# Kernel tuning notes

Hardware: AMD Instinct MI355X
Metric: run time of the kernel (lower is better)

Reference implementation:

```python
import jax, jax.numpy as jnp
import numpy as np

B, T, N_ITEMS, DIM, L = 512, 50, 10000, 128, 4
H = DIM // 2


def setup_inputs() -> dict:
    key = jax.random.key(0)
    ks = jax.random.split(key, 16)
    emb = jax.random.normal(ks[0], (N_ITEMS + 1, DIM), jnp.float32) * 0.02
    emb = emb.at[0].set(0.0)  # padding_idx=0
    s = 1.0 / np.sqrt(DIM)
    inp = {
        "users": jax.random.randint(ks[1], (B,), 0, B),
        "user_seq": jax.random.randint(ks[2], (B, T), 0, N_ITEMS + 1),
        "pos_items": jax.random.randint(ks[3], (B,), 0, N_ITEMS),
        "neg_items": jax.random.randint(ks[4], (B, 10), 0, N_ITEMS),
        "pos_labels": jnp.ones((B,), jnp.float32),
        "neg_labels": jnp.zeros((B, 10), jnp.float32),
        "base_model_preds": jax.random.normal(ks[5], (B, N_ITEMS), jnp.float32),
        "emb": emb,
        "lstm_wih": jax.random.uniform(ks[6], (4 * DIM, DIM), jnp.float32, -s, s),
        "lstm_whh": jax.random.uniform(ks[7], (4 * DIM, DIM), jnp.float32, -s, s),
        "lstm_bih": jax.random.uniform(ks[8], (4 * DIM,), jnp.float32, -s, s),
        "lstm_bhh": jax.random.uniform(ks[9], (4 * DIM,), jnp.float32, -s, s),
        "wl_W1": jax.random.normal(ks[10], (L, 2 * DIM, H), jnp.float32) * 0.05,
        "wl_b1": jax.random.normal(ks[11], (L, H), jnp.float32) * 0.01,
        "wl_W2": jax.random.normal(ks[12], (L, H), jnp.float32) * 0.05,
        "wl_b2": jax.random.normal(ks[13], (L,), jnp.float32) * 0.01,
        "alphas": jnp.ones((L,), jnp.float32) / L,
    }
    return inp


def _lstm_last(x, wih, whh, bih, bhh):
    # x: [B, T, D]; torch gate order i, f, g, o. Returns last hidden state [B, D].
    Bx, _, D = x.shape
    bias = bih + bhh

    def step(carry, xt):
        h, c = carry
        gates = xt @ wih.T + h @ whh.T + bias  # [B, 4D]
        i, f, g, o = jnp.split(gates, 4, axis=-1)
        c = jax.nn.sigmoid(f) * c + jax.nn.sigmoid(i) * jnp.tanh(g)
        h = jax.nn.sigmoid(o) * jnp.tanh(c)
        return (h, c), None

    init = (jnp.zeros((Bx, D), x.dtype), jnp.zeros((Bx, D), x.dtype))
    (h, _), _ = jax.lax.scan(step, init, x.transpose(1, 0, 2))
    return h


def reference(users, user_seq, pos_items, neg_items, pos_labels, neg_labels,
              base_model_preds, emb, lstm_wih, lstm_whh, lstm_bih, lstm_bhh,
              wl_W1, wl_b1, wl_W2, wl_b2, alphas):
    seq_emb = emb[user_seq]                      # [B, T, D]
    seq_repr = _lstm_last(seq_emb, lstm_wih, lstm_whh, lstm_bih, lstm_bhh)  # [B, D]
    item_emb = emb[jnp.arange(N_ITEMS)]          # [N, D]

    # Weak learners: Linear(2D->H) split algebraically into seq/item matmuls
    # to avoid materializing the [B, N, 2D] broadcast-concat tensor.
    final_scores = jnp.zeros((seq_repr.shape[0], N_ITEMS), seq_repr.dtype)
    for l in range(L):
        sp = seq_repr @ wl_W1[l, :DIM]           # [B, H]
        ip = item_emb @ wl_W1[l, DIM:]           # [N, H]
        hid = jax.nn.relu(sp[:, None, :] + ip[None, :, :] + wl_b1[l])  # [B, N, H]
        scores = hid @ wl_W2[l] + wl_b2[l]       # [B, N]
        final_scores = final_scores + alphas[l] * scores

    pos_scores = jnp.take_along_axis(final_scores, pos_items[:, None], axis=1)  # [B, 1]
    neg_scores = jnp.take_along_axis(final_scores, neg_items, axis=1)           # [B, n_neg]
    loss = jnp.mean(jnp.exp(-(pos_scores - neg_scores)))
    return final_scores, loss
```

## Files before the change

kernel.cpp:

```cpp
#include <hip/hip_runtime.h>
#include <stdint.h>

typedef uint32_t u32;
typedef uint16_t u16;
typedef uint64_t u64;
typedef __attribute__((ext_vector_type(4))) float f32x4;
typedef __attribute__((ext_vector_type(8))) short bf16x8;
typedef __attribute__((ext_vector_type(2))) _Float16 f16x2;

#define NI   10000
#define NPAD 10240
#define L2E  1.4426950408889634f

#define DEV static __device__ __forceinline__

DEV float asf(u32 u){ union{u32 i; float f;} v; v.i=u; return v.f; }
DEV u32   asu(float f){ union{u32 i; float f;} v; v.f=f; return v.i; }
DEV float bf2f(u16 u){ return asf(((u32)u)<<16); }
DEV u16   f2bf(float f){ u32 i = asu(f); return (u16)((i + 0x7fffu + ((i>>16)&1u))>>16); }
DEV u16   f2h(float f){ _Float16 h = (_Float16)f; return __builtin_bit_cast(u16, h); }
DEV f32x4 fzero(){ f32x4 z; z[0]=0.f; z[1]=0.f; z[2]=0.f; z[3]=0.f; return z; }

DEV void gl2lds16(const void* g, void* l){
  __builtin_amdgcn_global_load_lds((const __attribute__((address_space(1))) u32*)g,
                                   (__attribute__((address_space(3))) u32*)l, 16, 0, 0);
}

__global__ void k_prep(const int* __restrict__ seq, const float* __restrict__ emb,
                       const float* __restrict__ wih, const float* __restrict__ bih,
                       const float* __restrict__ bhh, const float* __restrict__ W1,
                       const float* __restrict__ b1, const float* __restrict__ W2,
                       const float* __restrict__ alphas,
                       u16* __restrict__ EMB16, u16* __restrict__ Wih16,
                       u16* __restrict__ W1s16, u16* __restrict__ W1i16,
                       float* __restrict__ bias512, float* __restrict__ b1k,
                       float* __restrict__ w2h, u32* __restrict__ w2p,
                       float* __restrict__ qv)
{
  const int tid = blockIdx.x*blockDim.x + threadIdx.x;
  const int nth = gridDim.x*blockDim.x;
  for (int e = tid; e < 10001*16; e += nth){
    const float* s = emb + (size_t)e*8;
    float4 x0 = *(const float4*)s, x1 = *(const float4*)(s+4);
    bf16x8 o;
    o[0]=(short)f2bf(x0.x); o[1]=(short)f2bf(x0.y); o[2]=(short)f2bf(x0.z); o[3]=(short)f2bf(x0.w);
    o[4]=(short)f2bf(x1.x); o[5]=(short)f2bf(x1.y); o[6]=(short)f2bf(x1.z); o[7]=(short)f2bf(x1.w);
    *(bf16x8*)&EMB16[(size_t)e*8] = o;
  }
  for (int e = tid; e < 512*16; e += nth){
    int col = (e*8)>>7;
    float sc = ((col>>7)==2) ? 2.0f*L2E : L2E;
    const float* s = wih + (size_t)e*8;
    float4 x0 = *(const float4*)s, x1 = *(const float4*)(s+4);
    bf16x8 o;
    o[0]=(short)f2bf(x0.x*sc); o[1]=(short)f2bf(x0.y*sc); o[2]=(short)f2bf(x0.z*sc); o[3]=(short)f2bf(x0.w*sc);
    o[4]=(short)f2bf(x1.x*sc); o[5]=(short)f2bf(x1.y*sc); o[6]=(short)f2bf(x1.z*sc); o[7]=(short)f2bf(x1.w*sc);
    *(bf16x8*)&Wih16[(size_t)e*8] = o;
  }
  for (int e = tid; e < 256*128; e += nth){ int k = e>>7, d = e&127; int l = k>>6, h = k&63;
      W1s16[e] = f2bf(W1[l*16384 + d*64 + h]); }
  for (int e = tid; e < 256*128; e += nth){ int k = e>>7, d = e&127; int l = k>>6, h = k&63;
      W1i16[e] = f2bf(W1[l*16384 + (128+d)*64 + h]); }
  for (int e = tid; e < 512; e += nth){
      float sc = ((e>>7)==2) ? 2.0f*L2E : L2E;
      bias512[e] = (bih[e] + bhh[e])*sc; }
  for (int e = tid; e < 256; e += nth){ int l = e>>6, h = e&63;
      b1k[e] = b1[l*64 + h]; w2h[e] = 0.5f*alphas[l]*W2[l*64 + h]; }
  for (int e = tid; e < 128; e += nth){
      int k0 = 2*e, k1 = 2*e+1;
      float w0 = 0.5f*alphas[k0>>6]*W2[(k0>>6)*64 + (k0&63)];
      float w1 = 0.5f*alphas[k1>>6]*W2[(k1>>6)*64 + (k1&63)];
      w2p[e] = (u32)f2h(w0) | ((u32)f2h(w1)<<16); }
  for (int d = tid; d < 128; d += nth){
    float s = 0.f;
    for (int k=0;k<256;++k){
      float wv = 0.5f*alphas[k>>6]*W2[(k>>6)*64 + (k&63)];
      s = fmaf(wv, W1[(k>>6)*16384 + d*64 + (k&63)], s);
    }
    qv[d] = s;
  }
}

template<int OUT_MODE, int BIAS_MODE>
DEV void gemm_body(const u16* __restrict__ A, const u16* __restrict__ BT,
                   const float* __restrict__ bias, void* __restrict__ Cout,
                   int Nvalid, int ldc, int bx, int by, char* smem,
                   const int* __restrict__ seq)
{
  u16* sA = (u16*)smem;
  u16* sB = (u16*)(smem + 32768);
  const int tid = threadIdx.x, l = tid&63, w = tid>>6;
  const int c16 = l&15, g4 = l>>4;
  const int m0 = bx*128, n0 = by*64;
  #pragma unroll
  for (int it=0; it<4; ++it){
    int row = it*32 + w*4 + g4;
    int sg  = c16 ^ (row&7);
    if constexpr (OUT_MODE==4){
      int b = (m0&511) + row, t = m0>>9;
      int idx = seq[b*50 + t];
      gl2lds16(A + (size_t)idx*128 + sg*8, (char*)sA + (it*32 + w*4)*256);
    } else {
      gl2lds16(A + (size_t)(m0+row)*128 + sg*8, (char*)sA + (it*32 + w*4)*256);
    }
  }
  #pragma unroll
  for (int it=0; it<2; ++it){
    int row = it*32 + w*4 + g4;
    int srow;
    if constexpr (OUT_MODE==4){
      int base1 = (by>>2)*256 + (by&3)*32;
      srow = base1 + (row&31) + (row>>5)*128;
    } else {
      srow = n0 + row; if (srow >= Nvalid) srow = Nvalid-1;
    }
    int sg  = c16 ^ (row&7);
    gl2lds16(BT + (size_t)srow*128 + sg*8, (char*)sB + (it*32 + w*4)*256);
  }
  __syncthreads();
  f32x4 acc[4];
  #pragma unroll
  for (int ct=0; ct<4; ++ct) acc[ct] = fzero();
  #pragma unroll
  for (int kt=0; kt<4; ++kt){
    bf16x8 a, b[4];
    int arow = w*16 + c16;
    a = *(const bf16x8*)((const char*)sA + arow*256 + (((kt*4+g4) ^ (arow&7))*16));
    #pragma unroll
    for (int ct=0; ct<4; ++ct){
      int brow = (OUT_MODE==4) ? ((ct>>1)*32 + (ct&1)*16 + c16) : (ct*16 + c16);
      b[ct] = *(const bf16x8*)((const char*)sB + brow*256 + (((kt*4+g4) ^ (brow&7))*16));
    }
    #pragma unroll
    for (int ct=0; ct<4; ++ct)
      acc[ct] = __builtin_amdgcn_mfma_f32_16x16x32_bf16(a, b[ct], acc[ct], 0, 0, 0);
  }
  const int rbase = m0 + w*16 + g4*4;
  if constexpr (OUT_MODE==4){
    int t    = rbase >> 9;
    int bloc = rbase & 511;
    int bb   = bloc >> 4;
    int g4l  = (bloc >> 2) & 3;
    int half = by >> 2;
    #pragma unroll
    for (int p=0; p<2; ++p){
      int colA = (by&3)*32 + p*16 + c16 + (by>>2)*256;
      int colB = colA + 128;
      u32 ws[4];
      #pragma unroll
      for (int i=0;i<4;++i){
        float va = acc[p][i], vb = acc[p+2][i];
        if constexpr (BIAS_MODE==1){ va += bias[colA]; vb += bias[colB]; }
        ws[i] = (u32)f2bf(va) | ((u32)f2bf(vb)<<16);
      }
      int tidl = ((by&3)*2 + p)*64 + g4l*16 + c16;
      char* dst = (char*)Cout + ((size_t)((t*32+bb)*1024 + half*512 + tidl))*16;
      *(f32x4*)dst = *(f32x4*)ws;
    }
  } else {
    #pragma unroll
    for (int ct=0; ct<4; ++ct){
      int col = n0 + ct*16 + c16;
      if (col < Nvalid){
        float v[4];
        #pragma unroll
        for (int i=0;i<4;++i){
          v[i] = acc[ct][i];
          if constexpr (BIAS_MODE==1) v[i] += bias[col];
          else if constexpr (BIAS_MODE==2) v[i] += bias[rbase+i];
        }
        if constexpr (OUT_MODE==0){
          float* C = (float*)Cout;
          #pragma unroll
          for (int i=0;i<4;++i) C[(size_t)(rbase+i)*ldc + col] = v[i];
        } else if constexpr (OUT_MODE==1){
          u16* C = (u16*)Cout;
          #pragma unroll
          for (int i=0;i<4;++i) C[(size_t)(rbase+i)*ldc + col] = f2h(v[i]);
        } else {
          u32* C = (u32*)Cout;
          u32 w0 = (u32)f2h(v[0]) | ((u32)f2h(v[1])<<16);
          u32 w1 = (u32)f2h(v[2]) | ((u32)f2h(v[3])<<16);
          int kp0 = rbase>>1;
          C[(size_t)kp0*ldc + col]     = w0;
          C[(size_t)(kp0+1)*ldc + col] = w1;
        }
      }
    }
  }
}

template<int OUT_MODE, int BIAS_MODE>
__global__ __launch_bounds__(512) void k_gemm(const u16* __restrict__ A,
    const u16* __restrict__ BT, const float* __restrict__ bias,
    void* __restrict__ Cout, int Nvalid, int ldc, const int* __restrict__ seq)
{
  __shared__ __align__(16) char smem[49152];
  gemm_body<OUT_MODE,BIAS_MODE>(A, BT, bias, Cout, Nvalid, ldc, blockIdx.x, blockIdx.y, smem, seq);
}

DEV void lstm_body(const float* __restrict__ whh, const u16* __restrict__ XWL,
                   u16* __restrict__ H16, int bb, char* smem)
{
  const int tid = threadIdx.x, l = tid&63, w = tid>>6;
  const int c16 = l&15, g4 = l>>4;
  const int u = w*16 + c16;
  bf16x8 bfr[4][4];
  #pragma unroll
  for (int j=0; j<4; ++j){
    int col = (j*8 + w)*16 + c16;
    float sc = (j==2) ? 2.0f*L2E : L2E;
    const float* src = whh + (size_t)col*128;
    #pragma unroll
    for (int kt=0; kt<4; ++kt){
      int k0 = kt*32 + g4*8;
      float4 x0 = *(const float4*)(src + k0);
      float4 x1 = *(const float4*)(src + k0 + 4);
      bf16x8 f;
      f[0]=(short)f2bf(x0.x*sc); f[1]=(short)f2bf(x0.y*sc); f[2]=(short)f2bf(x0.z*sc); f[3]=(short)f2bf(x0.w*sc);
      f[4]=(short)f2bf(x1.x*sc); f[5]=(short)f2bf(x1.y*sc); f[6]=(short)f2bf(x1.z*sc); f[7]=(short)f2bf(x1.w*sc);
      bfr[kt][j] = f;
    }
  }
  for (int e = tid; e < 4096; e += 512) ((u16*)smem)[e] = 0;
  int hoff[4];
  #pragma unroll
  for (int i=0;i<4;++i){ int s = g4*4 + i;
    hoff[i] = s*256 + (((u>>3) ^ (s&7))*16) + (u&7)*2; }
  const char* gb = (const char*)XWL;
  {
    size_t base = (size_t)bb*1024;
    gl2lds16(gb + (base + tid)*16,        smem + 8192 + w*1024);
    gl2lds16(gb + (base + 512 + tid)*16,  smem + 8192 + 8192 + w*1024);
  }
  float cst[4] = {0.f,0.f,0.f,0.f};
  float hreg[4] = {0.f,0.f,0.f,0.f};
  __syncthreads();
  #pragma unroll 2
  for (int t=0; t<50; ++t){
    const int cur = t&1;
    char* AhC = smem + cur*4096;
    char* AhN = smem + (cur^1)*4096;
    char* XsC = smem + 8192 + cur*16384;
    char* XsN = smem + 8192 + (cur^1)*16384;
    if (t < 49){
      size_t base = (size_t)((t+1)*32+bb)*1024;
      gl2lds16(gb + (base + tid)*16,       XsN + w*1024);
      gl2lds16(gb + (base + 512 + tid)*16, XsN + 8192 + w*1024);
    }
    bf16x8 xv0 = *(const bf16x8*)(XsC + tid*16);
    bf16x8 xv1 = *(const bf16x8*)(XsC + 8192 + tid*16);
    const u32* W0 = (const u32*)&xv0;
    const u32* W1 = (const u32*)&xv1;
    f32x4 acc[4];
    #pragma unroll
    for (int i=0;i<4;++i){
      acc[0][i] = asf(W0[i]<<16);
      acc[1][i] = asf(W0[i]&0xffff0000u);
      acc[2][i] = asf(W1[i]<<16);
      acc[3][i] = asf(W1[i]&0xffff0000u);
    }
    #pragma unroll
    for (int kt=0; kt<4; ++kt){
      bf16x8 a = *(const bf16x8*)(AhC + c16*256 + (((kt*4+g4) ^ (c16&7))*16));
      #pragma unroll
      for (int j=0; j<4; ++j)
        acc[j] = __builtin_amdgcn_mfma_f32_16x16x32_bf16(a, bfr[kt][j], acc[j], 0, 0, 0);
    }
    #pragma unroll
    for (int i=0;i<4;++i){
      float yi = acc[0][i], yf = acc[1][i], yg = acc[2][i], yo = acc[3][i];
      yg = fminf(fmaxf(yg, -40.f), 40.f);
      float Ei = __builtin_amdgcn_exp2f(-yi);
      float Ef = __builtin_amdgcn_exp2f(-yf);
      float G  = __builtin_amdgcn_exp2f(yg);
      float Eo = __builtin_amdgcn_exp2f(-yo);
      float ai = 1.f+Ei, af = 1.f+Ef, gp = G+1.f, gm = G-1.f;
      float num = fmaf(af, gm, cst[i]*ai*gp);
      float den = af*ai*gp;
      float cn  = num * __builtin_amdgcn_rcpf(den);
      cst[i] = cn;
      float yc = fminf(fmaxf(cn*(2.0f*L2E), -40.f), 40.f);
      float C2 = __builtin_amdgcn_exp2f(yc);
      float h  = (C2-1.f) * __builtin_amdgcn_rcpf((1.f+Eo)*(C2+1.f));
      hreg[i] = h;
      *(u16*)(AhN + hoff[i]) = f2bf(h);
    }
    __syncthreads();
  }
  #pragma unroll
  for (int i=0;i<4;++i)
    H16[(size_t)(bb*16 + g4*4 + i)*128 + u] = f2bf(hreg[i]);
}

__global__ __launch_bounds__(512) void k_lstm_ipf(const float* __restrict__ whh,
    const u16* __restrict__ XWL, u16* __restrict__ H16,
    const u16* __restrict__ W1i16, const u16* __restrict__ EMB16,
    const float* __restrict__ b1k, u32* __restrict__ IPF)
{
  __shared__ __align__(16) char smem[49152];
  if (blockIdx.x < 32){
    lstm_body(whh, XWL, H16, blockIdx.x, smem);
  } else {
    int g = blockIdx.x - 32;
    gemm_body<2,2>(W1i16, EMB16, b1k, IPF, NI, NPAD, g&1, g>>1, smem, nullptr);
  }
}

__global__ __launch_bounds__(512) void k_post(const u16* __restrict__ H16,
    const u16* __restrict__ W1s16, u16* __restrict__ SPH,
    const float* __restrict__ qv, float* __restrict__ cB,
    const u32* __restrict__ IPF, const float* __restrict__ b2,
    const float* __restrict__ alphas, const float* __restrict__ w2h,
    float* __restrict__ cN)
{
  __shared__ __align__(16) char smem[49152];
  const int bid = blockIdx.x;
  if (bid < 16){
    gemm_body<1,0>(H16, W1s16, nullptr, SPH, 256, 256, bid&3, bid>>2, smem, nullptr);
  } else if (bid == 16){
    int b = threadIdx.x;
    float s = 0.f;
    #pragma unroll
    for (int d8=0; d8<16; ++d8){
      bf16x8 hv = *(const bf16x8*)&H16[(size_t)b*128 + d8*8];
      #pragma unroll
      for (int j=0;j<8;++j) s = fmaf(bf2f((u16)hv[j]), qv[d8*8+j], s);
    }
    cB[b] = s;
  } else {
    int n = (bid-17)*512 + threadIdx.x;
    if (n >= NPAD) return;
    if (n >= NI){ cN[n] = 0.f; return; }
    float cb2 = 0.f;
    #pragma unroll
    for (int l=0;l<4;++l) cb2 += alphas[l]*b2[l];
    float s = cb2;
    for (int kp=0; kp<128; ++kp){
      f16x2 h = __builtin_bit_cast(f16x2, IPF[(size_t)kp*NPAD + n]);
      s = fmaf((float)h.x, w2h[2*kp],   s);
      s = fmaf((float)h.y, w2h[2*kp+1], s);
    }
    cN[n] = s;
  }
}

DEV float fdot2(u32 ab, u32 w, float acc){
  asm("v_dot2_f32_f16 %0, %1, %2, %0" : "+v"(acc) : "v"(ab), "s"(w));
  return acc;
}

__global__ __launch_bounds__(256) void k_score(const u32* __restrict__ SPH,
    const u32* __restrict__ IPF, const u32* __restrict__ w2p,
    const float* __restrict__ cB, const float* __restrict__ cN,
    float* __restrict__ out)
{
  const int n  = blockIdx.x*256 + threadIdx.x;
  const int b0 = blockIdx.y*8;
  const float cNv = cN[n];
  float acc[8];
  #pragma unroll
  for (int i=0;i<8;++i) acc[i] = cB[b0+i] + cNv;
  #pragma unroll 1
  for (int c=0;c<4;++c){
    u32 iw[32];
    #pragma unroll
    for (int v=0; v<32; ++v) iw[v] = IPF[(size_t)(c*32+v)*NPAD + n];
    const u32* wp = w2p + c*32;
    #pragma unroll
    for (int i=0;i<8;++i){
      const u32* sp = SPH + (size_t)(b0+i)*128 + c*32;
      float a = acc[i];
      #pragma unroll
      for (int v=0; v<32; ++v){
        f16x2 t = __builtin_bit_cast(f16x2, sp[v]) + __builtin_bit_cast(f16x2, iw[v]);
        u32 ta = __builtin_bit_cast(u32, t) & 0x7fff7fffu;
        a = fdot2(ta, wp[v], a);
      }
      acc[i] = a;
    }
  }
  if (n < NI){
    #pragma unroll
    for (int i=0;i<8;++i) out[(size_t)(b0+i)*NI + n] = acc[i];
  }
}

__global__ void k_loss(const float* __restrict__ scores, const int* __restrict__ pos,
                       const int* __restrict__ neg, float* __restrict__ outloss)
{
  __shared__ float red[256];
  int tid = threadIdx.x;
  float s = 0.f;
  for (int e = tid; e < 5120; e += 256){
    int b = e/10, j = e - b*10;
    float ps = scores[(size_t)b*NI + pos[b]];
    float ns = scores[(size_t)b*NI + neg[b*10 + j]];
    s += __expf(ns - ps);
  }
  red[tid] = s; __syncthreads();
  for (int st=128; st>0; st>>=1){ if (tid<st) red[tid]+=red[tid+st]; __syncthreads(); }
  if (tid==0) outloss[0] = red[0] * (1.0f/5120.0f);
}

extern "C" void kernel_launch(void* const* d_in, const int* in_sizes, int n_in,
                              void* d_out, int out_size, void* d_ws, size_t ws_size,
                              hipStream_t stream)
{
  const int*   seq    = (const int*)d_in[1];
  const int*   pos    = (const int*)d_in[2];
  const int*   neg    = (const int*)d_in[3];
  const float* emb    = (const float*)d_in[7];
  const float* wih    = (const float*)d_in[8];
  const float* whh    = (const float*)d_in[9];
  const float* bih    = (const float*)d_in[10];
  const float* bhh    = (const float*)d_in[11];
  const float* W1     = (const float*)d_in[12];
  const float* b1     = (const float*)d_in[13];
  const float* W2     = (const float*)d_in[14];
  const float* b2     = (const float*)d_in[15];
  const float* alphas = (const float*)d_in[16];
  float* out = (float*)d_out;
  (void)in_sizes; (void)n_in; (void)out_size; (void)ws_size;

  char* p = (char*)d_ws;
  size_t off = 0;
  auto alloc = [&](size_t bytes)->char*{ char* r = p + off;
      off = (off + bytes + 255) & ~(size_t)255; return r; };
  u16*  EMB16   = (u16*)  alloc((size_t)10001*128*2);
  u16*  Wih16   = (u16*)  alloc((size_t)512*128*2);
  u16*  W1s16   = (u16*)  alloc((size_t)256*128*2);
  u16*  W1i16   = (u16*)  alloc((size_t)256*128*2);
  float* bias512= (float*)alloc(512*4);
  float* b1k    = (float*)alloc(256*4);
  float* w2h    = (float*)alloc(256*4);
  u32*  w2p     = (u32*)  alloc(128*4);
  float* qv     = (float*)alloc(128*4);
  u16*  XWL     = (u16*)  alloc((size_t)25600*512*2);
  u16*  H16     = (u16*)  alloc((size_t)512*128*2);
  u16*  SPH     = (u16*)  alloc((size_t)512*256*2);
  u32*  IPF     = (u32*)  alloc((size_t)128*NPAD*4);
  float* cB     = (float*)alloc(512*4);
  float* cN     = (float*)alloc((size_t)NPAD*4);

  k_prep<<<512,256,0,stream>>>(seq, emb, wih, bih, bhh, W1, b1, W2, alphas,
                               EMB16, Wih16, W1s16, W1i16, bias512, b1k, w2h, w2p, qv);
  k_gemm<4,1><<<dim3(200,8),512,0,stream>>>(EMB16, Wih16, bias512, XWL, 512, 512, seq);
  k_lstm_ipf<<<32 + 314,512,0,stream>>>(whh, XWL, H16, W1i16, EMB16, b1k, IPF);
  k_post<<<37,512,0,stream>>>(H16, W1s16, SPH, qv, cB, IPF, b2, alphas, w2h, cN);
  k_score<<<dim3(40,64),256,0,stream>>>((const u32*)SPH, IPF, w2p, cB, cN, out);
  k_loss<<<1,256,0,stream>>>(out, pos, neg, out + (size_t)512*NI);
}
```

Before: 184.0 us.

## Replace abs-relu identity with packed max and tile 16 users per score block

The scoring kernel used to compute relu through the identity relu(x) = 0.5*(x+|x|), which needed per-user and per-item linear correction terms (cB, cN) computed in k_post and k_prep. It now applies relu directly with v_pk_max_f16 against zero and uses unhalved weights, so those correction computations and buffers are removed. k_score also handles 16 users per block instead of 8, staging the user projections in LDS, which halves how often the IPF item data is re-read. The cost is more accumulator registers per thread and one LDS staging step with a barrier; removing the cancellation between the two correction terms may also change numerical error slightly.

```diff
diff --git a/kernel.cpp b/kernel.cpp
--- a/kernel.cpp
+++ b/kernel.cpp
@@ -5,6 +5,7 @@
 typedef uint16_t u16;
 typedef uint64_t u64;
 typedef __attribute__((ext_vector_type(4))) float f32x4;
+typedef __attribute__((ext_vector_type(4))) u32 u32x4;
 typedef __attribute__((ext_vector_type(8))) short bf16x8;
 typedef __attribute__((ext_vector_type(2))) _Float16 f16x2;
 
@@ -34,8 +35,7 @@
                        u16* __restrict__ EMB16, u16* __restrict__ Wih16,
                        u16* __restrict__ W1s16, u16* __restrict__ W1i16,
                        float* __restrict__ bias512, float* __restrict__ b1k,
-                       float* __restrict__ w2h, u32* __restrict__ w2p,
-                       float* __restrict__ qv)
+                       u32* __restrict__ w2p)
 {
   const int tid = blockIdx.x*blockDim.x + threadIdx.x;
   const int nth = gridDim.x*blockDim.x;
@@ -65,20 +65,12 @@
       float sc = ((e>>7)==2) ? 2.0f*L2E : L2E;
       bias512[e] = (bih[e] + bhh[e])*sc; }
   for (int e = tid; e < 256; e += nth){ int l = e>>6, h = e&63;
-      b1k[e] = b1[l*64 + h]; w2h[e] = 0.5f*alphas[l]*W2[l*64 + h]; }
+      b1k[e] = b1[l*64 + h]; }
   for (int e = tid; e < 128; e += nth){
       int k0 = 2*e, k1 = 2*e+1;
-      float w0 = 0.5f*alphas[k0>>6]*W2[(k0>>6)*64 + (k0&63)];
-      float w1 = 0.5f*alphas[k1>>6]*W2[(k1>>6)*64 + (k1&63)];
+      float w0 = alphas[k0>>6]*W2[(k0>>6)*64 + (k0&63)];
+      float w1 = alphas[k1>>6]*W2[(k1>>6)*64 + (k1&63)];
       w2p[e] = (u32)f2h(w0) | ((u32)f2h(w1)<<16); }
-  for (int d = tid; d < 128; d += nth){
-    float s = 0.f;
-    for (int k=0;k<256;++k){
-      float wv = 0.5f*alphas[k>>6]*W2[(k>>6)*64 + (k&63)];
-      s = fmaf(wv, W1[(k>>6)*16384 + d*64 + (k&63)], s);
-    }
-    qv[d] = s;
-  }
 }
 
 template<int OUT_MODE, int BIAS_MODE>
@@ -308,59 +300,41 @@
 }
 
 __global__ __launch_bounds__(512) void k_post(const u16* __restrict__ H16,
-    const u16* __restrict__ W1s16, u16* __restrict__ SPH,
-    const float* __restrict__ qv, float* __restrict__ cB,
-    const u32* __restrict__ IPF, const float* __restrict__ b2,
-    const float* __restrict__ alphas, const float* __restrict__ w2h,
-    float* __restrict__ cN)
+    const u16* __restrict__ W1s16, u16* __restrict__ SPH)
 {
   __shared__ __align__(16) char smem[49152];
-  const int bid = blockIdx.x;
-  if (bid < 16){
-    gemm_body<1,0>(H16, W1s16, nullptr, SPH, 256, 256, bid&3, bid>>2, smem, nullptr);
-  } else if (bid == 16){
-    int b = threadIdx.x;
-    float s = 0.f;
-    #pragma unroll
-    for (int d8=0; d8<16; ++d8){
-      bf16x8 hv = *(const bf16x8*)&H16[(size_t)b*128 + d8*8];
-      #pragma unroll
-      for (int j=0;j<8;++j) s = fmaf(bf2f((u16)hv[j]), qv[d8*8+j], s);
-    }
-    cB[b] = s;
-  } else {
-    int n = (bid-17)*512 + threadIdx.x;
-    if (n >= NPAD) return;
-    if (n >= NI){ cN[n] = 0.f; return; }
-    float cb2 = 0.f;
-    #pragma unroll
-    for (int l=0;l<4;++l) cb2 += alphas[l]*b2[l];
-    float s = cb2;
-    for (int kp=0; kp<128; ++kp){
-      f16x2 h = __builtin_bit_cast(f16x2, IPF[(size_t)kp*NPAD + n]);
-      s = fmaf((float)h.x, w2h[2*kp],   s);
-      s = fmaf((float)h.y, w2h[2*kp+1], s);
-    }
-    cN[n] = s;
-  }
+  gemm_body<1,0>(H16, W1s16, nullptr, SPH, 256, 256, blockIdx.x&3, blockIdx.x>>2, smem, nullptr);
 }
 
 DEV float fdot2(u32 ab, u32 w, float acc){
   asm("v_dot2_f32_f16 %0, %1, %2, %0" : "+v"(acc) : "v"(ab), "s"(w));
   return acc;
 }
+DEV u32 pkmax0(u32 t){
+  u32 r; asm("v_pk_max_f16 %0, %1, 0" : "=v"(r) : "v"(t)); return r;
+}
 
 __global__ __launch_bounds__(256) void k_score(const u32* __restrict__ SPH,
     const u32* __restrict__ IPF, const u32* __restrict__ w2p,
-    const float* __restrict__ cB, const float* __restrict__ cN,
+    const float* __restrict__ alphas, const float* __restrict__ b2,
     float* __restrict__ out)
 {
-  const int n  = blockIdx.x*256 + threadIdx.x;
-  const int b0 = blockIdx.y*8;
-  const float cNv = cN[n];
-  float acc[8];
-  #pragma unroll
-  for (int i=0;i<8;++i) acc[i] = cB[b0+i] + cNv;
+  __shared__ __align__(16) u32 sp_lds[16*128];
+  const int tid = threadIdx.x;
+  const int n  = blockIdx.x*256 + tid;
+  const int b0 = blockIdx.y*16;
+  {
+    const u32* src = SPH + (size_t)b0*128 + tid*8;
+    *(u32x4*)&sp_lds[tid*8]   = *(const u32x4*)src;
+    *(u32x4*)&sp_lds[tid*8+4] = *(const u32x4*)(src+4);
+  }
+  float cb2 = 0.f;
+  #pragma unroll
+  for (int ll=0;ll<4;++ll) cb2 += alphas[ll]*b2[ll];
+  __syncthreads();
+  float acc[16];
+  #pragma unroll
+  for (int i=0;i<16;++i) acc[i] = cb2;
   #pragma unroll 1
   for (int c=0;c<4;++c){
     u32 iw[32];
@@ -368,21 +342,24 @@
     for (int v=0; v<32; ++v) iw[v] = IPF[(size_t)(c*32+v)*NPAD + n];
     const u32* wp = w2p + c*32;
     #pragma unroll
-    for (int i=0;i<8;++i){
-      const u32* sp = SPH + (size_t)(b0+i)*128 + c*32;
+    for (int i=0;i<16;++i){
       float a = acc[i];
       #pragma unroll
-      for (int v=0; v<32; ++v){
-        f16x2 t = __builtin_bit_cast(f16x2, sp[v]) + __builtin_bit_cast(f16x2, iw[v]);
-        u32 ta = __builtin_bit_cast(u32, t) & 0x7fff7fffu;
-        a = fdot2(ta, wp[v], a);
+      for (int vq=0; vq<8; ++vq){
+        u32x4 sp4 = *(const u32x4*)&sp_lds[i*128 + c*32 + vq*4];
+        #pragma unroll
+        for (int q=0;q<4;++q){
+          f16x2 t = __builtin_bit_cast(f16x2, sp4[q]) + __builtin_bit_cast(f16x2, iw[vq*4+q]);
+          u32 r = pkmax0(__builtin_bit_cast(u32, t));
+          a = fdot2(r, wp[vq*4+q], a);
+        }
       }
       acc[i] = a;
     }
   }
   if (n < NI){
     #pragma unroll
-    for (int i=0;i<8;++i) out[(size_t)(b0+i)*NI + n] = acc[i];
+    for (int i=0;i<16;++i) out[(size_t)(b0+i)*NI + n] = acc[i];
   }
 }
 
@@ -433,21 +410,17 @@
   u16*  W1i16   = (u16*)  alloc((size_t)256*128*2);
   float* bias512= (float*)alloc(512*4);
   float* b1k    = (float*)alloc(256*4);
-  float* w2h    = (float*)alloc(256*4);
   u32*  w2p     = (u32*)  alloc(128*4);
-  float* qv     = (float*)alloc(128*4);
   u16*  XWL     = (u16*)  alloc((size_t)25600*512*2);
   u16*  H16     = (u16*)  alloc((size_t)512*128*2);
   u16*  SPH     = (u16*)  alloc((size_t)512*256*2);
   u32*  IPF     = (u32*)  alloc((size_t)128*NPAD*4);
-  float* cB     = (float*)alloc(512*4);
-  float* cN     = (float*)alloc((size_t)NPAD*4);
 
   k_prep<<<512,256,0,stream>>>(seq, emb, wih, bih, bhh, W1, b1, W2, alphas,
-                               EMB16, Wih16, W1s16, W1i16, bias512, b1k, w2h, w2p, qv);
+                               EMB16, Wih16, W1s16, W1i16, bias512, b1k, w2p);
   k_gemm<4,1><<<dim3(200,8),512,0,stream>>>(EMB16, Wih16, bias512, XWL, 512, 512, seq);
   k_lstm_ipf<<<32 + 314,512,0,stream>>>(whh, XWL, H16, W1i16, EMB16, b1k, IPF);
-  k_post<<<37,512,0,stream>>>(H16, W1s16, SPH, qv, cB, IPF, b2, alphas, w2h, cN);
-  k_score<<<dim3(40,64),256,0,stream>>>((const u32*)SPH, IPF, w2p, cB, cN, out);
+  k_post<<<16,512,0,stream>>>(H16, W1s16, SPH);
+  k_score<<<dim3(40,32),256,0,stream>>>((const u32*)SPH, IPF, w2p, alphas, b2, out);
   k_loss<<<1,256,0,stream>>>(out, pos, neg, out + (size_t)512*NI);
 }
```

Measured after the change: 164.7 us. 1.12x faster.

## Switch score kernel from packed f16 dot2 to fp32 FMA with 16-row tiles

Applied to the files above, without the earlier changes.

Replaces the packed f16 add/abs/dot2 inner loop with fp32 add and FMA using the abs modifier, storing the seq projection in fp32 in a blocked layout. Each thread now handles 16 batch rows, halving reloads of the item projections. This improves accuracy and reuse, but roughly doubles the ALU instructions per element compared with packed half math.

```diff
diff --git a/kernel.cpp b/kernel.cpp
--- a/kernel.cpp
+++ b/kernel.cpp
@@ -5,6 +5,7 @@
 typedef uint16_t u16;
 typedef uint64_t u64;
 typedef __attribute__((ext_vector_type(4))) float f32x4;
+typedef __attribute__((ext_vector_type(4))) u32 u32x4;
 typedef __attribute__((ext_vector_type(8))) short bf16x8;
 typedef __attribute__((ext_vector_type(2))) _Float16 f16x2;
 
@@ -19,6 +20,7 @@
 DEV float bf2f(u16 u){ return asf(((u32)u)<<16); }
 DEV u16   f2bf(float f){ u32 i = asu(f); return (u16)((i + 0x7fffu + ((i>>16)&1u))>>16); }
 DEV u16   f2h(float f){ _Float16 h = (_Float16)f; return __builtin_bit_cast(u16, h); }
+DEV f16x2 h2c(u32 x){ return __builtin_bit_cast(f16x2, x); }
 DEV f32x4 fzero(){ f32x4 z; z[0]=0.f; z[1]=0.f; z[2]=0.f; z[3]=0.f; return z; }
 
 DEV void gl2lds16(const void* g, void* l){
@@ -34,8 +36,7 @@
                        u16* __restrict__ EMB16, u16* __restrict__ Wih16,
                        u16* __restrict__ W1s16, u16* __restrict__ W1i16,
                        float* __restrict__ bias512, float* __restrict__ b1k,
-                       float* __restrict__ w2h, u32* __restrict__ w2p,
-                       float* __restrict__ qv)
+                       float* __restrict__ w2hf, float* __restrict__ qv)
 {
   const int tid = blockIdx.x*blockDim.x + threadIdx.x;
   const int nth = gridDim.x*blockDim.x;
@@ -65,12 +66,9 @@
       float sc = ((e>>7)==2) ? 2.0f*L2E : L2E;
       bias512[e] = (bih[e] + bhh[e])*sc; }
   for (int e = tid; e < 256; e += nth){ int l = e>>6, h = e&63;
-      b1k[e] = b1[l*64 + h]; w2h[e] = 0.5f*alphas[l]*W2[l*64 + h]; }
-  for (int e = tid; e < 128; e += nth){
-      int k0 = 2*e, k1 = 2*e+1;
-      float w0 = 0.5f*alphas[k0>>6]*W2[(k0>>6)*64 + (k0&63)];
-      float w1 = 0.5f*alphas[k1>>6]*W2[(k1>>6)*64 + (k1&63)];
-      w2p[e] = (u32)f2h(w0) | ((u32)f2h(w1)<<16); }
+      b1k[e] = b1[l*64 + h]; }
+  for (int e = tid; e < 256; e += nth)
+      w2hf[e] = 0.5f*alphas[e>>6]*W2[(e>>6)*64 + (e&63)];
   for (int d = tid; d < 128; d += nth){
     float s = 0.f;
     for (int k=0;k<256;++k){
@@ -173,10 +171,15 @@
           float* C = (float*)Cout;
           #pragma unroll
           for (int i=0;i<4;++i) C[(size_t)(rbase+i)*ldc + col] = v[i];
-        } else if constexpr (OUT_MODE==1){
-          u16* C = (u16*)Cout;
+        } else if constexpr (OUT_MODE==6){
+          float* C = (float*)Cout;
+          int kc = col>>4, kin = col&15;
           #pragma unroll
-          for (int i=0;i<4;++i) C[(size_t)(rbase+i)*ldc + col] = f2h(v[i]);
+          for (int i=0;i<4;++i){
+            int b = rbase + i;
+            size_t adr = (((size_t)(b>>4)*16 + kc)*16 + (b&15))*16 + kin;
+            C[adr] = v[i];
+          }
         } else {
           u32* C = (u32*)Cout;
           u32 w0 = (u32)f2h(v[0]) | ((u32)f2h(v[1])<<16);
@@ -308,16 +311,16 @@
 }
 
 __global__ __launch_bounds__(512) void k_post(const u16* __restrict__ H16,
-    const u16* __restrict__ W1s16, u16* __restrict__ SPH,
+    const u16* __restrict__ W1s16, float* __restrict__ SPf,
     const float* __restrict__ qv, float* __restrict__ cB,
     const u32* __restrict__ IPF, const float* __restrict__ b2,
-    const float* __restrict__ alphas, const float* __restrict__ w2h,
+    const float* __restrict__ alphas, const float* __restrict__ w2hf,
     float* __restrict__ cN)
 {
   __shared__ __align__(16) char smem[49152];
   const int bid = blockIdx.x;
   if (bid < 16){
-    gemm_body<1,0>(H16, W1s16, nullptr, SPH, 256, 256, bid&3, bid>>2, smem, nullptr);
+    gemm_body<6,0>(H16, W1s16, nullptr, SPf, 256, 256, bid&3, bid>>2, smem, nullptr);
   } else if (bid == 16){
     int b = threadIdx.x;
     float s = 0.f;
@@ -334,55 +337,62 @@
     if (n >= NI){ cN[n] = 0.f; return; }
     float cb2 = 0.f;
     #pragma unroll
-    for (int l=0;l<4;++l) cb2 += alphas[l]*b2[l];
+    for (int ll=0;ll<4;++ll) cb2 += alphas[ll]*b2[ll];
     float s = cb2;
     for (int kp=0; kp<128; ++kp){
-      f16x2 h = __builtin_bit_cast(f16x2, IPF[(size_t)kp*NPAD + n]);
-      s = fmaf((float)h.x, w2h[2*kp],   s);
-      s = fmaf((float)h.y, w2h[2*kp+1], s);
+      f16x2 h = h2c(IPF[(size_t)kp*NPAD + n]);
+      s = fmaf((float)h.x, w2hf[2*kp],   s);
+      s = fmaf((float)h.y, w2hf[2*kp+1], s);
     }
     cN[n] = s;
   }
 }
 
-DEV float fdot2(u32 ab, u32 w, float acc){
-  asm("v_dot2_f32_f16 %0, %1, %2, %0" : "+v"(acc) : "v"(ab), "s"(w));
-  return acc;
-}
-
-__global__ __launch_bounds__(256) void k_score(const u32* __restrict__ SPH,
-    const u32* __restrict__ IPF, const u32* __restrict__ w2p,
+__global__ __launch_bounds__(256) void k_score(const float* __restrict__ SPf,
+    const u32* __restrict__ IPF, const float* __restrict__ w2hf,
     const float* __restrict__ cB, const float* __restrict__ cN,
     float* __restrict__ out)
 {
-  const int n  = blockIdx.x*256 + threadIdx.x;
-  const int b0 = blockIdx.y*8;
+  const int tid = threadIdx.x;
+  const int n  = blockIdx.x*256 + tid;
+  const int btile = blockIdx.y;
+  const int b0 = btile*16;
   const float cNv = cN[n];
-  float acc[8];
-  #pragma unroll
-  for (int i=0;i<8;++i) acc[i] = cB[b0+i] + cNv;
+  float acc[16];
+  #pragma unroll
+  for (int i=0;i<16;++i) acc[i] = cB[b0+i] + cNv;
   #pragma unroll 1
-  for (int c=0;c<4;++c){
-    u32 iw[32];
-    #pragma unroll
-    for (int v=0; v<32; ++v) iw[v] = IPF[(size_t)(c*32+v)*NPAD + n];
-    const u32* wp = w2p + c*32;
-    #pragma unroll
-    for (int i=0;i<8;++i){
-      const u32* sp = SPH + (size_t)(b0+i)*128 + c*32;
+  for (int kc=0; kc<16; ++kc){
+    u32 ipw[8];
+    #pragma unroll
+    for (int j=0;j<8;++j) ipw[j] = IPF[(size_t)(kc*8+j)*NPAD + n];
+    float ipf[16];
+    #pragma unroll
+    for (int j=0;j<8;++j){
+      f16x2 h = h2c(ipw[j]);
+      ipf[2*j]   = (float)h.x;
+      ipf[2*j+1] = (float)h.y;
+    }
+    const float* w2c = w2hf + kc*16;
+    float w2v[16];
+    #pragma unroll
+    for (int k=0;k<16;++k) w2v[k] = w2c[k];
+    const float* spB = SPf + ((size_t)btile*16 + kc)*256;
+    #pragma unroll
+    for (int i=0;i<16;++i){
+      const float* sp = spB + i*16;
       float a = acc[i];
       #pragma unroll
-      for (int v=0; v<32; ++v){
-        f16x2 t = __builtin_bit_cast(f16x2, sp[v]) + __builtin_bit_cast(f16x2, iw[v]);
-        u32 ta = __builtin_bit_cast(u32, t) & 0x7fff7fffu;
-        a = fdot2(ta, wp[v], a);
+      for (int k=0;k<16;++k){
+        float t = sp[k] + ipf[k];
+        a = fmaf(fabsf(t), w2v[k], a);
       }
       acc[i] = a;
     }
   }
   if (n < NI){
     #pragma unroll
-    for (int i=0;i<8;++i) out[(size_t)(b0+i)*NI + n] = acc[i];
+    for (int i=0;i<16;++i) out[(size_t)(b0+i)*NI + n] = acc[i];
   }
 }
 
@@ -433,21 +443,20 @@
   u16*  W1i16   = (u16*)  alloc((size_t)256*128*2);
   float* bias512= (float*)alloc(512*4);
   float* b1k    = (float*)alloc(256*4);
-  float* w2h    = (float*)alloc(256*4);
-  u32*  w2p     = (u32*)  alloc(128*4);
+  float* w2hf   = (float*)alloc(256*4);
   float* qv     = (float*)alloc(128*4);
   u16*  XWL     = (u16*)  alloc((size_t)25600*512*2);
   u16*  H16     = (u16*)  alloc((size_t)512*128*2);
-  u16*  SPH     = (u16*)  alloc((size_t)512*256*2);
+  float* SPf    = (float*)alloc((size_t)512*256*4);
   u32*  IPF     = (u32*)  alloc((size_t)128*NPAD*4);
   float* cB     = (float*)alloc(512*4);
   float* cN     = (float*)alloc((size_t)NPAD*4);
 
   k_prep<<<512,256,0,stream>>>(seq, emb, wih, bih, bhh, W1, b1, W2, alphas,
-                               EMB16, Wih16, W1s16, W1i16, bias512, b1k, w2h, w2p, qv);
+                               EMB16, Wih16, W1s16, W1i16, bias512, b1k, w2hf, qv);
   k_gemm<4,1><<<dim3(200,8),512,0,stream>>>(EMB16, Wih16, bias512, XWL, 512, 512, seq);
   k_lstm_ipf<<<32 + 314,512,0,stream>>>(whh, XWL, H16, W1i16, EMB16, b1k, IPF);
-  k_post<<<37,512,0,stream>>>(H16, W1s16, SPH, qv, cB, IPF, b2, alphas, w2h, cN);
-  k_score<<<dim3(40,64),256,0,stream>>>((const u32*)SPH, IPF, w2p, cB, cN, out);
+  k_post<<<37,512,0,stream>>>(H16, W1s16, SPf, qv, cB, IPF, b2, alphas, w2hf, cN);
+  k_score<<<dim3(40,32),256,0,stream>>>(SPf, IPF, w2hf, cB, cN, out);
   k_loss<<<1,256,0,stream>>>(out, pos, neg, out + (size_t)512*NI);
 }
```

After: 208.5 us. 1.13x slower.
